# Kernel tuning notes

Measured on AMD Instinct MI355X. Metric: run time of the kernel, lower is better.

Reference implementation:

```python
import jax, jax.numpy as jnp
import numpy as np

B, S, D, H = 2, 2048, 2048, 16
HD = D // H  # head_dim = 128

def _rope_tables(head_dim, context_length, theta_base=10000.0):
    inv_freq = 1.0 / theta_base ** (jnp.arange(0, head_dim, 2, dtype=jnp.float32) / head_dim)
    pos = jnp.arange(context_length, dtype=jnp.float32)
    angles = pos[:, None] * inv_freq[None, :]            # [S, HD/2]
    angles = jnp.concatenate([angles, angles], axis=1)   # [S, HD]
    return jnp.cos(angles), jnp.sin(angles)

def _apply_rope(x, cos, sin):
    # x: [b, h, s, hd]; cos/sin: [s, hd]
    hd = x.shape[-1]
    x1, x2 = x[..., : hd // 2], x[..., hd // 2 :]
    rotated = jnp.concatenate([-x2, x1], axis=-1)
    return x * cos[None, None] + rotated * sin[None, None]

def setup_inputs() -> dict:
    key = jax.random.key(0)
    ks = jax.random.split(key, 5)
    x = jax.random.normal(ks[0], (B, S, D), dtype=jnp.float32)
    scale = 1.0 / np.sqrt(D)
    Wq = jax.random.normal(ks[1], (D, D), dtype=jnp.float32) * scale
    Wk = jax.random.normal(ks[2], (D, D), dtype=jnp.float32) * scale
    Wv = jax.random.normal(ks[3], (D, D), dtype=jnp.float32) * scale
    Wo = jax.random.normal(ks[4], (D, D), dtype=jnp.float32) * scale
    cos, sin = _rope_tables(HD, S)
    return {"x": x, "Wq": Wq, "Wk": Wk, "Wv": Wv, "Wo": Wo, "cos": cos, "sin": sin}

def reference(x, Wq, Wk, Wv, Wo, cos, sin):
    b, s, _ = x.shape
    def split_heads(t):  # [b,s,D] -> [b,H,s,HD]
        return t.reshape(b, s, H, HD).transpose(0, 2, 1, 3)
    q = split_heads(x @ Wq.T)
    k = split_heads(x @ Wk.T)
    v = split_heads(x @ Wv.T)
    q = _apply_rope(q, cos[:s], sin[:s])
    k = _apply_rope(k, cos[:s], sin[:s])
    scores = jnp.einsum("bhqd,bhkd->bhqk", q, k) / np.sqrt(HD)
    causal = jnp.triu(jnp.ones((s, s), dtype=bool), k=1)
    scores = jnp.where(causal[None, None], -jnp.inf, scores)
    weights = jax.nn.softmax(scores, axis=-1)
    ctx = jnp.einsum("bhqk,bhkd->bhqd", weights, v)
    ctx = ctx.transpose(0, 2, 1, 3).reshape(b, s, D)
    return ctx @ Wo.T
```

## Files before the change

### kernel.cpp

```cpp
#include <hip/hip_runtime.h>
#include <cstdint>
#include <cmath>

#define B_ 2
#define S_ 2048
#define D_ 2048
#define H_ 16
#define HD_ 128

#define NEG_SENTINEL -1.0e30f

typedef __bf16 bf16;
typedef __attribute__((ext_vector_type(4))) __bf16 bf16x4;
typedef __attribute__((ext_vector_type(8))) __bf16 bf16x8;
typedef __attribute__((ext_vector_type(4))) float f32x4;

__device__ __forceinline__ void gload_lds16(const void* g, void* l) {
  __builtin_amdgcn_global_load_lds(
      (const __attribute__((address_space(1))) unsigned int*)g,
      (__attribute__((address_space(3))) unsigned int*)l, 16, 0, 0);
}

__device__ __forceinline__ f32x4 mfma16(bf16x8 a, bf16x8 b, f32x4 c) {
  return __builtin_amdgcn_mfma_f32_16x16x32_bf16(a, b, c, 0, 0, 0);
}

__device__ __forceinline__ void wg_barrier() {
  asm volatile("" ::: "memory");
  __builtin_amdgcn_s_barrier();
  asm volatile("" ::: "memory");
}

#define AVM0() asm volatile("s_waitcnt vmcnt(0)" ::: "memory")

__global__ __launch_bounds__(256) void cvt_f32_bf16(
    const float* __restrict__ in, bf16* __restrict__ out)
{
  int i = blockIdx.x * 256 + threadIdx.x;
  f32x4 v = ((const f32x4*)in)[i];
  bf16x4 o;
#pragma unroll
  for (int j = 0; j < 4; ++j) o[j] = (bf16)v[j];
  ((bf16x4*)out)[i] = o;
}

__global__ __launch_bounds__(256) void cvt_qkvx(
    const float* __restrict__ x, bf16* __restrict__ xb,
    const float* __restrict__ wq, const float* __restrict__ wk,
    const float* __restrict__ wv, bf16* __restrict__ wout)
{
  int b = (int)blockIdx.x;
  const float* in; bf16* out; int base;
  if (b < 8192)      { in = x;  out = xb; base = b; }
  else {
    int r = b - 8192; int j = r >> 12; base = r & 4095;
    if (j == 0)      { in = wq; out = wout; }
    else if (j == 1) { in = wk; out = wout + 4194304; }
    else             { in = wv; out = wout + 8388608; }
  }
  int i = base * 256 + threadIdx.x;
  f32x4 v = ((const f32x4*)in)[i];
  bf16x4 o;
#pragma unroll
  for (int t2 = 0; t2 < 4; ++t2) o[t2] = (bf16)v[t2];
  ((bf16x4*)out)[i] = o;
}

#define GTM 128
#define GTN 128
#define GBK 64

template <typename OT>
__global__ __launch_bounds__(256) void gemm_xwt(
    const bf16* __restrict__ A, const bf16* __restrict__ W, OT* __restrict__ C,
    int M, int N, int K, int ldc)
{
  __shared__ bf16 sA[GTM * GBK];
  __shared__ bf16 sB[GTN * GBK];
  const int tid  = threadIdx.x;
  const int wave = tid >> 6, lane = tid & 63;
  const int quad = lane >> 4, l16 = lane & 15;
  const int tm = blockIdx.y * GTM;
  const int tn = blockIdx.x * GTN;
  const int wm = (wave >> 1) * 64, wn = (wave & 1) * 64;

  f32x4 acc[4][4];
#pragma unroll
  for (int i = 0; i < 4; ++i)
#pragma unroll
    for (int j = 0; j < 4; ++j) acc[i][j] = (f32x4)0.0f;

  for (int k0 = 0; k0 < K; k0 += GBK) {
    __syncthreads();
#pragma unroll
    for (int g = 0; g < 4; ++g) {
      int gb  = (g * 4 + wave) * 64;
      int p   = gb + lane;
      int row = p >> 3, pos = p & 7;
      int cc  = pos ^ (row & 7);
      gload_lds16(A + (size_t)(tm + row) * K + k0 + cc * 8, (char*)sA + (size_t)gb * 16);
      gload_lds16(W + (size_t)(tn + row) * K + k0 + cc * 8, (char*)sB + (size_t)gb * 16);
    }
    __syncthreads();

#pragma unroll
    for (int t = 0; t < 2; ++t) {
      bf16x8 af[4], bfr[4];
#pragma unroll
      for (int i = 0; i < 4; ++i) {
        int rowa = wm + i * 16 + l16;
        int posa = (t * 4 + quad) ^ (rowa & 7);
        af[i] = *(const bf16x8*)(sA + rowa * GBK + posa * 8);
        int rowb = wn + i * 16 + l16;
        int posb = (t * 4 + quad) ^ (rowb & 7);
        bfr[i] = *(const bf16x8*)(sB + rowb * GBK + posb * 8);
      }
#pragma unroll
      for (int i = 0; i < 4; ++i)
#pragma unroll
        for (int j = 0; j < 4; ++j)
          acc[i][j] = mfma16(af[i], bfr[j], acc[i][j]);
    }
  }

#pragma unroll
  for (int i = 0; i < 4; ++i)
#pragma unroll
    for (int r = 0; r < 4; ++r) {
      int row = tm + wm + i * 16 + quad * 4 + r;
#pragma unroll
      for (int j = 0; j < 4; ++j) {
        int col = tn + wn + j * 16 + l16;
        C[(size_t)row * ldc + col] = (OT)acc[i][j][r];
      }
    }
}

__global__ __launch_bounds__(256) void rope_qk(
    bf16* __restrict__ Q, bf16* __restrict__ Kk,
    const float* __restrict__ cosT, const float* __restrict__ sinT, int rs)
{
  const float kappa = 0.08838834764831845f * 1.4426950408889634f;
  int t  = blockIdx.x * 256 + threadIdx.x;
  int d0 = (t & 7) * 8;
  int h  = (t >> 3) & (H_ - 1);
  int s  = (t >> 7) & (S_ - 1);
  int b  = t >> 18;
  size_t base = ((size_t)(b * S_ + s)) * rs + (size_t)h * HD_;

  const float* cl = cosT + s * HD_ + d0;
  const float* sl = sinT + s * HD_ + d0;

  bf16x8 ql = *(const bf16x8*)(Q + base + d0);
  bf16x8 qh = *(const bf16x8*)(Q + base + 64 + d0);
  bf16x8 kl = *(const bf16x8*)(Kk + base + d0);
  bf16x8 kh = *(const bf16x8*)(Kk + base + 64 + d0);

  bf16x8 qlo, qho, klo, kho;
#pragma unroll
  for (int i = 0; i < 8; ++i) {
    float c1 = cl[i], s1 = sl[i];
    float c2 = cl[64 + i], s2 = sl[64 + i];
    float x1 = (float)ql[i], x2 = (float)qh[i];
    qlo[i] = (bf16)((x1 * c1 - x2 * s1) * kappa);
    qho[i] = (bf16)((x2 * c2 + x1 * s2) * kappa);
    float y1 = (float)kl[i], y2 = (float)kh[i];
    klo[i] = (bf16)(y1 * c1 - y2 * s1);
    kho[i] = (bf16)(y2 * c2 + y1 * s2);
  }
  *(bf16x8*)(Q + base + d0)       = qlo;
  *(bf16x8*)(Q + base + 64 + d0)  = qho;
  *(bf16x8*)(Kk + base + d0)      = klo;
  *(bf16x8*)(Kk + base + 64 + d0) = kho;
}

__global__ __launch_bounds__(256) void transpose_v(
    const bf16* __restrict__ V, bf16* __restrict__ Vt, int rs)
{
  __shared__ bf16 sT[64 * 72];
  const int tid = threadIdx.x;
  const int si = blockIdx.x;
  const int di = blockIdx.y;
  const int bh = blockIdx.z;
  const int b  = bh >> 4, h = bh & 15;

  const bf16* src = V + (size_t)b * S_ * rs + (size_t)h * HD_ + di * 64;
  bf16*       dst = Vt + ((size_t)bh * HD_ + di * 64) * S_ + si * 64;

#pragma unroll
  for (int half = 0; half < 2; ++half) {
    int r  = half * 32 + (tid >> 3);
    int c0 = (tid & 7) * 8;
    bf16x8 v = *(const bf16x8*)(src + (size_t)(si * 64 + r) * rs + c0);
    *(bf16x8*)(sT + r * 72 + c0) = v;
  }
  __syncthreads();
#pragma unroll
  for (int half = 0; half < 2; ++half) {
    int dr = half * 32 + (tid >> 3);
    int c0 = (tid & 7) * 8;
    bf16x8 o;
#pragma unroll
    for (int j = 0; j < 8; ++j) o[j] = sT[(c0 + j) * 72 + dr];
    *(bf16x8*)(dst + (size_t)dr * S_ + c0) = o;
  }
}

#define ABK 64
#define SPS 72

#define AK_STAGE(kt_, b_) do { \
    int kk_ = (kt_) * ABK; \
    _Pragma("unroll") \
    for (int g_ = 0; g_ < 2; ++g_) { \
      int p_   = g_ * 512 + tid; \
      int row_ = p_ >> 4, pos_ = p_ & 15; \
      int cc_  = pos_ ^ (row_ & 15); \
      gload_lds16(Kh + (size_t)(kk_ + row_) * rs + cc_ * 8, \
                  (char*)sK + (b_) * 16384 + (size_t)p_ * 16); \
    } } while (0)

#define AV_STAGE(kt_, b_) do { \
    int kk_ = (kt_) * ABK; \
    _Pragma("unroll") \
    for (int g_ = 0; g_ < 2; ++g_) { \
      int p_  = g_ * 512 + tid; \
      int d_  = p_ >> 3, pos_ = p_ & 7; \
      int cc_ = pos_ ^ (d_ & 7); \
      gload_lds16(Vth + (size_t)d_ * S_ + kk_ + cc_ * 8, \
                  (char*)sVT + (b_) * 16384 + (size_t)p_ * 16); \
    } } while (0)

__global__ __launch_bounds__(512) void attn_fwd(
    const bf16* __restrict__ Q, const bf16* __restrict__ K,
    const bf16* __restrict__ Vt, bf16* __restrict__ O, int rs)
{
  __shared__ bf16 sK[2 * ABK * HD_];
  __shared__ bf16 sVT[2 * HD_ * ABK];
  __shared__ bf16 sP[128 * SPS];

  const int tid  = threadIdx.x;
  const int wave = tid >> 6, lane = tid & 63;
  const int quad = lane >> 4, l16 = lane & 15;

  const int lin   = (int)blockIdx.x;
  const int low3  = lin & 7;
  const int rest  = lin >> 3;
  const int pairx = rest & 7;
  const int colhi = rest >> 3;
  const int col   = low3 + (colhi << 3);
  const int b = col >> 4, h = col & 15;

  const bf16* Qh  = Q + (size_t)b * S_ * rs + (size_t)h * HD_;
  const bf16* Kh  = K + (size_t)b * S_ * rs + (size_t)h * HD_;
  const bf16* Vth = Vt + ((size_t)(b * H_ + h) * HD_) * S_;
  bf16*       Oh  = O + (size_t)b * S_ * D_ + (size_t)h * HD_;

  const int wq = wave * 16;

#pragma unroll 1
  for (int seg = 0; seg < 2; ++seg) {
    const int qt = seg == 0 ? pairx : 15 - pairx;
    const int q0 = qt * 128;
    const int wq_abs = q0 + wq;

    bf16x8 qf[4];
    {
      const bf16* rp = Qh + (size_t)(wq_abs + l16) * rs + quad * 8;
#pragma unroll
      for (int t = 0; t < 4; ++t) qf[t] = *(const bf16x8*)(rp + t * 32);
    }

    f32x4 o_acc[8];
#pragma unroll
    for (int j = 0; j < 8; ++j) o_acc[j] = (f32x4)0.0f;
    float m_col = NEG_SENTINEL;
    float l_col = 0.0f;

    const int nkt = 2 * qt + 2;

    AK_STAGE(0, 0);
    AV_STAGE(0, 0);
    AVM0();
    wg_barrier();

    int cur = 0;
#pragma unroll 1
    for (int kt = 0; kt < nkt; ++kt) {
      const int kk0 = kt * ABK;
      const bf16* sKc = sK + cur * (ABK * HD_);
      const bf16* sVc = sVT + cur * (HD_ * ABK);

      if (kt + 1 < nkt) {
        AK_STAGE(kt + 1, cur ^ 1);
        AV_STAGE(kt + 1, cur ^ 1);
      }

      if (kk0 <= wq_abs + 15) {
        f32x4 st[4];
#pragma unroll
        for (int jt = 0; jt < 4; ++jt) {
          bf16x8 kf[4];
#pragma unroll
          for (int t = 0; t < 4; ++t) {
            int pos = (t * 4 + quad) ^ l16;
            kf[t] = *(const bf16x8*)(sKc + (jt * 16 + l16) * HD_ + pos * 8);
          }
          f32x4 a2 = (f32x4)0.0f;
#pragma unroll
          for (int t = 0; t < 4; ++t) a2 = mfma16(kf[t], qf[t], a2);
          st[jt] = a2;
        }

        if (kk0 + 63 > wq_abs) {
          int qcol = wq_abs + l16;
#pragma unroll
          for (int jt = 0; jt < 4; ++jt)
#pragma unroll
            for (int r = 0; r < 4; ++r) {
              int key = kk0 + jt * 16 + quad * 4 + r;
              if (key > qcol) st[jt][r] = NEG_SENTINEL;
            }
        }

        float mx = NEG_SENTINEL;
#pragma unroll
        for (int jt = 0; jt < 4; ++jt)
#pragma unroll
          for (int r = 0; r < 4; ++r) mx = fmaxf(mx, st[jt][r]);
        mx = fmaxf(mx, __shfl_xor(mx, 16, 64));
        mx = fmaxf(mx, __shfl_xor(mx, 32, 64));
        float m_new = fmaxf(m_col, mx);
        float alpha = exp2f(m_col - m_new);
        float ts = 0.0f;
#pragma unroll
        for (int jt = 0; jt < 4; ++jt) {
          bf16x4 pk;
#pragma unroll
          for (int r = 0; r < 4; ++r) {
            float p = exp2f(st[jt][r] - m_new);
            ts += p;
            pk[r] = (bf16)p;
          }
          *(bf16x4*)(sP + (wq + l16) * SPS + jt * 16 + quad * 4) = pk;
        }
        ts += __shfl_xor(ts, 16, 64);
        ts += __shfl_xor(ts, 32, 64);
        l_col = l_col * alpha + ts;
        m_col = m_new;
#pragma unroll
        for (int r = 0; r < 4; ++r) {
          float av = __shfl(alpha, quad * 4 + r, 64);
#pragma unroll
          for (int jd = 0; jd < 8; ++jd) o_acc[jd][r] *= av;
        }

#pragma unroll
        for (int ks = 0; ks < 2; ++ks) {
          bf16x8 pf = *(const bf16x8*)(sP + (wq + l16) * SPS + ks * 32 + quad * 8);
#pragma unroll
          for (int jd = 0; jd < 8; ++jd) {
            int pos = (ks * 4 + quad) ^ (l16 & 7);
            bf16x8 vf = *(const bf16x8*)(sVc + (jd * 16 + l16) * ABK + pos * 8);
            o_acc[jd] = mfma16(pf, vf, o_acc[jd]);
          }
        }
      }

      AVM0();
      wg_barrier();
      cur ^= 1;
    }

#pragma unroll
    for (int r = 0; r < 4; ++r) {
      float lv = __shfl(l_col, quad * 4 + r, 64);
      float inv_l = 1.0f / lv;
      int row = wq_abs + quad * 4 + r;
#pragma unroll
      for (int jd = 0; jd < 8; ++jd) {
        int colo = jd * 16 + l16;
        Oh[(size_t)row * D_ + colo] = (bf16)(o_acc[jd][r] * inv_l);
      }
    }
  }
}

extern "C" void kernel_launch(void* const* d_in, const int* in_sizes, int n_in,
                              void* d_out, int out_size, void* d_ws, size_t ws_size,
                              hipStream_t stream) {
  const float* x    = (const float*)d_in[0];
  const float* Wq   = (const float*)d_in[1];
  const float* Wk   = (const float*)d_in[2];
  const float* Wv   = (const float*)d_in[3];
  const float* Wo   = (const float*)d_in[4];
  const float* cosT = (const float*)d_in[5];
  const float* sinT = (const float*)d_in[6];
  float* out = (float*)d_out;

  const size_t NE = (size_t)B_ * S_ * D_;
  const size_t WE = (size_t)D_ * D_;
  const int M = B_ * S_;
  const int cvtX = (int)(NE / 1024);
  const int cvtW = (int)(WE / 1024);
  const int ropeG = (B_ * S_ * H_ * 8) / 256;

  if (ws_size >= (size_t)92274688) {
    bf16* QKV   = (bf16*)d_ws;
    bf16* xb    = QKV + (size_t)M * 6144;
    bf16* Wqkv  = xb + NE;
    bf16* ctx   = Wqkv;
    bf16* Wob   = Wqkv + 2 * WE;
    bf16* Vt    = xb;

    cvt_qkvx<<<8192 + 3 * 4096, 256, 0, stream>>>(x, xb, Wq, Wk, Wv, Wqkv);
    gemm_xwt<bf16><<<dim3(48, 32), 256, 0, stream>>>(xb, Wqkv, QKV, M, 3 * D_, D_, 3 * D_);
    rope_qk<<<ropeG, 256, 0, stream>>>(QKV, QKV + D_, cosT, sinT, 3 * D_);
    transpose_v<<<dim3(32, 2, 32), 256, 0, stream>>>(QKV + 2 * D_, Vt, 3 * D_);
    attn_fwd<<<256, 512, 0, stream>>>(QKV, QKV + D_, Vt, ctx, 3 * D_);
    cvt_f32_bf16<<<cvtW, 256, 0, stream>>>(Wo, Wob);
    gemm_xwt<float><<<dim3(16, 32), 256, 0, stream>>>(ctx, Wob, out, M, D_, D_, D_);
  } else {
    bf16* Qb    = (bf16*)d_ws;
    bf16* Kb    = Qb + NE;
    bf16* Vb    = Kb + NE;
    bf16* Cb    = Vb + NE;
    bf16* Wslot = Cb + NE;

    cvt_f32_bf16<<<cvtX, 256, 0, stream>>>(x, Cb);
    cvt_f32_bf16<<<cvtW, 256, 0, stream>>>(Wq, Wslot);
    gemm_xwt<bf16><<<dim3(16, 32), 256, 0, stream>>>(Cb, Wslot, Qb, M, D_, D_, D_);
    cvt_f32_bf16<<<cvtW, 256, 0, stream>>>(Wk, Wslot);
    gemm_xwt<bf16><<<dim3(16, 32), 256, 0, stream>>>(Cb, Wslot, Kb, M, D_, D_, D_);
    cvt_f32_bf16<<<cvtW, 256, 0, stream>>>(Wv, Wslot);
    gemm_xwt<bf16><<<dim3(16, 32), 256, 0, stream>>>(Cb, Wslot, Vb, M, D_, D_, D_);
    rope_qk<<<ropeG, 256, 0, stream>>>(Qb, Kb, cosT, sinT, D_);
    transpose_v<<<dim3(32, 2, 32), 256, 0, stream>>>(Vb, Cb, D_);
    attn_fwd<<<256, 512, 0, stream>>>(Qb, Kb, Cb, Vb, D_);
    cvt_f32_bf16<<<cvtW, 256, 0, stream>>>(Wo, Wslot);
    gemm_xwt<float><<<dim3(16, 32), 256, 0, stream>>>(Vb, Wslot, out, M, D_, D_, D_);
  }
}
```

Measured before the change: 379.8 us.

## Split attention q-tile pairs into separate blocks and single-buffer V loads

The attention kernel now launches 512 blocks with one 128-row query tile each, instead of 256 blocks that each looped over a mirrored pair of tiles. K stays double-buffered, while V is single-buffered and loaded at the start of each iteration, so it overlaps with QK^T and softmax. A partial vmcnt wait and an extra barrier separate the softmax phase from the PV matmul. Shared memory moves to a dynamic allocation of about 66 KB. More blocks should fill the CUs better and the smaller LDS footprint may allow more residency, at the cost of losing the causal load balancing the tile pairing gave and adding a second barrier per iteration.

```diff
diff --git a/kernel.cpp b/kernel.cpp
--- a/kernel.cpp
+++ b/kernel.cpp
@@ -32,6 +32,7 @@
 }
 
 #define AVM0() asm volatile("s_waitcnt vmcnt(0)" ::: "memory")
+#define AVM2() asm volatile("s_waitcnt vmcnt(2)" ::: "memory")
 
 __global__ __launch_bounds__(256) void cvt_f32_bf16(
     const float* __restrict__ in, bf16* __restrict__ out)
@@ -208,6 +209,7 @@
 
 #define ABK 64
 #define SPS 72
+#define ALDS 67584
 
 #define AK_STAGE(kt_, b_) do { \
     int kk_ = (kt_) * ABK; \
@@ -217,10 +219,10 @@
       int row_ = p_ >> 4, pos_ = p_ & 15; \
       int cc_  = pos_ ^ (row_ & 15); \
       gload_lds16(Kh + (size_t)(kk_ + row_) * rs + cc_ * 8, \
-                  (char*)sK + (b_) * 16384 + (size_t)p_ * 16); \
+                  smem + (b_) * 16384 + (size_t)p_ * 16); \
     } } while (0)
 
-#define AV_STAGE(kt_, b_) do { \
+#define AV_STAGE(kt_) do { \
     int kk_ = (kt_) * ABK; \
     _Pragma("unroll") \
     for (int g_ = 0; g_ < 2; ++g_) { \
@@ -228,26 +230,30 @@
       int d_  = p_ >> 3, pos_ = p_ & 7; \
       int cc_ = pos_ ^ (d_ & 7); \
       gload_lds16(Vth + (size_t)d_ * S_ + kk_ + cc_ * 8, \
-                  (char*)sVT + (b_) * 16384 + (size_t)p_ * 16); \
+                  smem + 32768 + (size_t)p_ * 16); \
     } } while (0)
 
 __global__ __launch_bounds__(512) void attn_fwd(
     const bf16* __restrict__ Q, const bf16* __restrict__ K,
     const bf16* __restrict__ Vt, bf16* __restrict__ O, int rs)
 {
-  __shared__ bf16 sK[2 * ABK * HD_];
-  __shared__ bf16 sVT[2 * HD_ * ABK];
-  __shared__ bf16 sP[128 * SPS];
+  extern __shared__ char smem[];
+  bf16* sK = (bf16*)smem;
+  bf16* sV = (bf16*)(smem + 32768);
+  bf16* sP = (bf16*)(smem + 49152);
 
   const int tid  = threadIdx.x;
   const int wave = tid >> 6, lane = tid & 63;
   const int quad = lane >> 4, l16 = lane & 15;
 
   const int lin   = (int)blockIdx.x;
-  const int low3  = lin & 7;
-  const int rest  = lin >> 3;
+  const int half  = lin >> 8;
+  const int l8    = lin & 255;
+  const int low3  = l8 & 7;
+  const int rest  = l8 >> 3;
   const int pairx = rest & 7;
   const int colhi = rest >> 3;
+  const int qt    = half ? pairx : 15 - pairx;
   const int col   = low3 + (colhi << 3);
   const int b = col >> 4, h = col & 15;
 
@@ -257,131 +263,128 @@
   bf16*       Oh  = O + (size_t)b * S_ * D_ + (size_t)h * HD_;
 
   const int wq = wave * 16;
-
+  const int q0 = qt * 128;
+  const int wq_abs = q0 + wq;
+
+  bf16x8 qf[4];
+  {
+    const bf16* rp = Qh + (size_t)(wq_abs + l16) * rs + quad * 8;
+#pragma unroll
+    for (int t = 0; t < 4; ++t) qf[t] = *(const bf16x8*)(rp + t * 32);
+  }
+
+  f32x4 o_acc[8];
+#pragma unroll
+  for (int j = 0; j < 8; ++j) o_acc[j] = (f32x4)0.0f;
+  float m_col = NEG_SENTINEL;
+  float l_col = 0.0f;
+
+  const int nkt = 2 * qt + 2;
+
+  AK_STAGE(0, 0);
+  AVM0();
+  wg_barrier();
+
+  int cur = 0;
 #pragma unroll 1
-  for (int seg = 0; seg < 2; ++seg) {
-    const int qt = seg == 0 ? pairx : 15 - pairx;
-    const int q0 = qt * 128;
-    const int wq_abs = q0 + wq;
-
-    bf16x8 qf[4];
-    {
-      const bf16* rp = Qh + (size_t)(wq_abs + l16) * rs + quad * 8;
-#pragma unroll
-      for (int t = 0; t < 4; ++t) qf[t] = *(const bf16x8*)(rp + t * 32);
-    }
-
-    f32x4 o_acc[8];
-#pragma unroll
-    for (int j = 0; j < 8; ++j) o_acc[j] = (f32x4)0.0f;
-    float m_col = NEG_SENTINEL;
-    float l_col = 0.0f;
-
-    const int nkt = 2 * qt + 2;
-
-    AK_STAGE(0, 0);
-    AV_STAGE(0, 0);
+  for (int kt = 0; kt < nkt; ++kt) {
+    const int kk0 = kt * ABK;
+    const bf16* sKc = sK + cur * (ABK * HD_);
+
+    AV_STAGE(kt);
+    const bool have_k = (kt + 1 < nkt);
+    if (have_k) AK_STAGE(kt + 1, cur ^ 1);
+
+    if (kk0 <= wq_abs + 15) {
+      f32x4 st[4];
+#pragma unroll
+      for (int jt = 0; jt < 4; ++jt) {
+        bf16x8 kf[4];
+#pragma unroll
+        for (int t = 0; t < 4; ++t) {
+          int pos = (t * 4 + quad) ^ l16;
+          kf[t] = *(const bf16x8*)(sKc + (jt * 16 + l16) * HD_ + pos * 8);
+        }
+        f32x4 a2 = (f32x4)0.0f;
+#pragma unroll
+        for (int t = 0; t < 4; ++t) a2 = mfma16(kf[t], qf[t], a2);
+        st[jt] = a2;
+      }
+
+      if (kk0 + 63 > wq_abs) {
+        int qcol = wq_abs + l16;
+#pragma unroll
+        for (int jt = 0; jt < 4; ++jt)
+#pragma unroll
+          for (int r = 0; r < 4; ++r) {
+            int key = kk0 + jt * 16 + quad * 4 + r;
+            if (key > qcol) st[jt][r] = NEG_SENTINEL;
+          }
+      }
+
+      float mx = NEG_SENTINEL;
+#pragma unroll
+      for (int jt = 0; jt < 4; ++jt)
+#pragma unroll
+        for (int r = 0; r < 4; ++r) mx = fmaxf(mx, st[jt][r]);
+      mx = fmaxf(mx, __shfl_xor(mx, 16, 64));
+      mx = fmaxf(mx, __shfl_xor(mx, 32, 64));
+      float m_new = fmaxf(m_col, mx);
+      float alpha = exp2f(m_col - m_new);
+      float ts = 0.0f;
+#pragma unroll
+      for (int jt = 0; jt < 4; ++jt) {
+        bf16x4 pk;
+#pragma unroll
+        for (int r = 0; r < 4; ++r) {
+          float p = exp2f(st[jt][r] - m_new);
+          ts += p;
+          pk[r] = (bf16)p;
+        }
+        *(bf16x4*)(sP + (wq + l16) * SPS + jt * 16 + quad * 4) = pk;
+      }
+      ts += __shfl_xor(ts, 16, 64);
+      ts += __shfl_xor(ts, 32, 64);
+      l_col = l_col * alpha + ts;
+      m_col = m_new;
+#pragma unroll
+      for (int r = 0; r < 4; ++r) {
+        float av = __shfl(alpha, quad * 4 + r, 64);
+#pragma unroll
+        for (int jd = 0; jd < 8; ++jd) o_acc[jd][r] *= av;
+      }
+    }
+
+    if (have_k) { AVM2(); } else { AVM0(); }
+    wg_barrier();
+
+    if (kk0 <= wq_abs + 15) {
+#pragma unroll
+      for (int ks = 0; ks < 2; ++ks) {
+        bf16x8 pf = *(const bf16x8*)(sP + (wq + l16) * SPS + ks * 32 + quad * 8);
+#pragma unroll
+        for (int jd = 0; jd < 8; ++jd) {
+          int pos = (ks * 4 + quad) ^ (l16 & 7);
+          bf16x8 vf = *(const bf16x8*)(sV + (jd * 16 + l16) * ABK + pos * 8);
+          o_acc[jd] = mfma16(pf, vf, o_acc[jd]);
+        }
+      }
+    }
+
     AVM0();
     wg_barrier();
-
-    int cur = 0;
-#pragma unroll 1
-    for (int kt = 0; kt < nkt; ++kt) {
-      const int kk0 = kt * ABK;
-      const bf16* sKc = sK + cur * (ABK * HD_);
-      const bf16* sVc = sVT + cur * (HD_ * ABK);
-
-      if (kt + 1 < nkt) {
-        AK_STAGE(kt + 1, cur ^ 1);
-        AV_STAGE(kt + 1, cur ^ 1);
-      }
-
-      if (kk0 <= wq_abs + 15) {
-        f32x4 st[4];
-#pragma unroll
-        for (int jt = 0; jt < 4; ++jt) {
-          bf16x8 kf[4];
-#pragma unroll
-          for (int t = 0; t < 4; ++t) {
-            int pos = (t * 4 + quad) ^ l16;
-            kf[t] = *(const bf16x8*)(sKc + (jt * 16 + l16) * HD_ + pos * 8);
-          }
-          f32x4 a2 = (f32x4)0.0f;
-#pragma unroll
-          for (int t = 0; t < 4; ++t) a2 = mfma16(kf[t], qf[t], a2);
-          st[jt] = a2;
-        }
-
-        if (kk0 + 63 > wq_abs) {
-          int qcol = wq_abs + l16;
-#pragma unroll
-          for (int jt = 0; jt < 4; ++jt)
-#pragma unroll
-            for (int r = 0; r < 4; ++r) {
-              int key = kk0 + jt * 16 + quad * 4 + r;
-              if (key > qcol) st[jt][r] = NEG_SENTINEL;
-            }
-        }
-
-        float mx = NEG_SENTINEL;
-#pragma unroll
-        for (int jt = 0; jt < 4; ++jt)
-#pragma unroll
-          for (int r = 0; r < 4; ++r) mx = fmaxf(mx, st[jt][r]);
-        mx = fmaxf(mx, __shfl_xor(mx, 16, 64));
-        mx = fmaxf(mx, __shfl_xor(mx, 32, 64));
-        float m_new = fmaxf(m_col, mx);
-        float alpha = exp2f(m_col - m_new);
-        float ts = 0.0f;
-#pragma unroll
-        for (int jt = 0; jt < 4; ++jt) {
-          bf16x4 pk;
-#pragma unroll
-          for (int r = 0; r < 4; ++r) {
-            float p = exp2f(st[jt][r] - m_new);
-            ts += p;
-            pk[r] = (bf16)p;
-          }
-          *(bf16x4*)(sP + (wq + l16) * SPS + jt * 16 + quad * 4) = pk;
-        }
-        ts += __shfl_xor(ts, 16, 64);
-        ts += __shfl_xor(ts, 32, 64);
-        l_col = l_col * alpha + ts;
-        m_col = m_new;
-#pragma unroll
-        for (int r = 0; r < 4; ++r) {
-          float av = __shfl(alpha, quad * 4 + r, 64);
-#pragma unroll
-          for (int jd = 0; jd < 8; ++jd) o_acc[jd][r] *= av;
-        }
-
-#pragma unroll
-        for (int ks = 0; ks < 2; ++ks) {
-          bf16x8 pf = *(const bf16x8*)(sP + (wq + l16) * SPS + ks * 32 + quad * 8);
-#pragma unroll
-          for (int jd = 0; jd < 8; ++jd) {
-            int pos = (ks * 4 + quad) ^ (l16 & 7);
-            bf16x8 vf = *(const bf16x8*)(sVc + (jd * 16 + l16) * ABK + pos * 8);
-            o_acc[jd] = mfma16(pf, vf, o_acc[jd]);
-          }
-        }
-      }
-
-      AVM0();
-      wg_barrier();
-      cur ^= 1;
-    }
-
-#pragma unroll
-    for (int r = 0; r < 4; ++r) {
-      float lv = __shfl(l_col, quad * 4 + r, 64);
-      float inv_l = 1.0f / lv;
-      int row = wq_abs + quad * 4 + r;
-#pragma unroll
-      for (int jd = 0; jd < 8; ++jd) {
-        int colo = jd * 16 + l16;
-        Oh[(size_t)row * D_ + colo] = (bf16)(o_acc[jd][r] * inv_l);
-      }
+    cur ^= 1;
+  }
+
+#pragma unroll
+  for (int r = 0; r < 4; ++r) {
+    float lv = __shfl(l_col, quad * 4 + r, 64);
+    float inv_l = 1.0f / lv;
+    int row = wq_abs + quad * 4 + r;
+#pragma unroll
+    for (int jd = 0; jd < 8; ++jd) {
+      int colo = jd * 16 + l16;
+      Oh[(size_t)row * D_ + colo] = (bf16)(o_acc[jd][r] * inv_l);
     }
   }
 }
@@ -405,6 +408,13 @@
   const int cvtW = (int)(WE / 1024);
   const int ropeG = (B_ * S_ * H_ * 8) / 256;
 
+  static bool attr_done = false;
+  if (!attr_done) {
+    (void)hipFuncSetAttribute(reinterpret_cast<const void*>(attn_fwd),
+                              hipFuncAttributeMaxDynamicSharedMemorySize, ALDS);
+    attr_done = true;
+  }
+
   if (ws_size >= (size_t)92274688) {
     bf16* QKV   = (bf16*)d_ws;
     bf16* xb    = QKV + (size_t)M * 6144;
@@ -417,7 +427,7 @@
     gemm_xwt<bf16><<<dim3(48, 32), 256, 0, stream>>>(xb, Wqkv, QKV, M, 3 * D_, D_, 3 * D_);
     rope_qk<<<ropeG, 256, 0, stream>>>(QKV, QKV + D_, cosT, sinT, 3 * D_);
     transpose_v<<<dim3(32, 2, 32), 256, 0, stream>>>(QKV + 2 * D_, Vt, 3 * D_);
-    attn_fwd<<<256, 512, 0, stream>>>(QKV, QKV + D_, Vt, ctx, 3 * D_);
+    attn_fwd<<<512, 512, ALDS, stream>>>(QKV, QKV + D_, Vt, ctx, 3 * D_);
     cvt_f32_bf16<<<cvtW, 256, 0, stream>>>(Wo, Wob);
     gemm_xwt<float><<<dim3(16, 32), 256, 0, stream>>>(ctx, Wob, out, M, D_, D_, D_);
   } else {
@@ -436,7 +446,7 @@
     gemm_xwt<bf16><<<dim3(16, 32), 256, 0, stream>>>(Cb, Wslot, Vb, M, D_, D_, D_);
     rope_qk<<<ropeG, 256, 0, stream>>>(Qb, Kb, cosT, sinT, D_);
     transpose_v<<<dim3(32, 2, 32), 256, 0, stream>>>(Vb, Cb, D_);
-    attn_fwd<<<256, 512, 0, stream>>>(Qb, Kb, Cb, Vb, D_);
+    attn_fwd<<<512, 512, ALDS, stream>>>(Qb, Kb, Cb, Vb, D_);
     cvt_f32_bf16<<<cvtW, 256, 0, stream>>>(Wo, Wslot);
     gemm_xwt<float><<<dim3(16, 32), 256, 0, stream>>>(Vb, Wslot, out, M, D_, D_, D_);
   }
```

New measurement: 380.1 us. No clear change (+0.1%).
